# Optimization experiments

Measured on AMD Instinct MI355X. Metric: run time of the kernel, lower is better.

Reference implementation:

```python
import jax, jax.numpy as jnp
import numpy as np

T = 32            # timesteps
DT = 1e-3
TAU_MEM_INV = 100.0   # norse LIFParameters / LIParameters default (1/1e-2)
TAU_SYN_INV = 200.0   # default (1/5e-3)
V_TH = 1.0
ALPHA = 100.0         # superspike surrogate slope

@jax.custom_vjp
def heaviside(x):
    return (x > 0).astype(x.dtype)

def _h_fwd(x):
    return heaviside(x), x

def _h_bwd(x, g):
    # superspike surrogate gradient
    return (g / (ALPHA * jnp.abs(x) + 1.0) ** 2,)

heaviside.defvjp(_h_fwd, _h_bwd)

LAYER_SIZES = [(2000, 12000), (1500, 2000), (1000, 1500), (500, 1000), (100, 500), (10, 100)]

def setup_inputs() -> dict:
    key = jax.random.key(0)
    ks = jax.random.split(key, 7)
    B = 128
    images = jax.random.normal(ks[0], (B, 3, 40, 100), dtype=jnp.float32)
    inp = {"images": images}
    for i, (out_f, in_f) in enumerate(LAYER_SIZES):
        scale = float(np.sqrt(2.0 / in_f))
        inp[f"w{i}"] = jax.random.normal(ks[i + 1], (out_f, in_f), dtype=jnp.float32) * scale
    return inp

def _encode(x):
    # norse ConstantCurrentLIFEncoder / lif_current_encode: voltage-only LIF
    def step(v, _):
        v = v + DT * TAU_MEM_INV * (-v + x)
        z = heaviside(v - V_TH)
        v = v - z * v  # v_reset = 0
        return v, z
    _, spikes = jax.lax.scan(step, jnp.zeros_like(x), None, length=T)
    return spikes  # [T, B, F]

def _lif_step(state, inp):
    # norse lif_feed_forward_step (parameter-free LIFCell)
    v, i = state
    v_dec = v + DT * TAU_MEM_INV * (-v + i)
    i_dec = i * (1.0 - DT * TAU_SYN_INV)
    z = heaviside(v_dec - V_TH)
    v_new = (1.0 - z) * v_dec  # v_reset = 0
    return (v_new, i_dec + inp), z

def _li_step(state, inp, w):
    # norse LILinearCell li_step (no bias)
    v, i = state
    i_jump = i + inp @ w.T
    v_new = v + DT * TAU_MEM_INV * (-v + i_jump)
    i_new = i_jump * (1.0 - DT * TAU_SYN_INV)
    return (v_new, i_new), v_new

def _forward(images, ws):
    B = images.shape[0]
    x = images.reshape(B, -1)  # [B, F]
    spikes = _encode(x)        # [T, B, F]
    lif_dims = [x.shape[1]] + [s[0] for s in LAYER_SIZES[:-1]]
    init_lif = tuple((jnp.zeros((B, d), x.dtype), jnp.zeros((B, d), x.dtype)) for d in lif_dims)
    init_li = tuple((jnp.zeros((B, s[0]), x.dtype), jnp.zeros((B, s[0]), x.dtype)) for s in LAYER_SIZES)

    def step(carry, s):
        lifs, lis = carry
        z = s
        new_lifs, new_lis = [], []
        for k in range(6):
            st, z = _lif_step(lifs[k], z)
            new_lifs.append(st)
            st2, z = _li_step(lis[k], z, ws[k])
            new_lis.append(st2)
        return (tuple(new_lifs), tuple(new_lis)), z

    _, outs = jax.lax.scan(step, (init_lif, init_li), spikes)  # [T, B, 10]
    out = jnp.max(outs, axis=0)
    return jax.nn.log_softmax(out, axis=1)

def reference(images, w0, w1, w2, w3, w4, w5):
    return _forward(images, (w0, w1, w2, w3, w4, w5))
```

## Files before the change

kernel.cpp:

```cpp
#include <hip/hip_runtime.h>

typedef _Float16 f16;
typedef _Float16 f16x2 __attribute__((ext_vector_type(2)));
typedef _Float16 f16x4 __attribute__((ext_vector_type(4)));
typedef _Float16 f16x8 __attribute__((ext_vector_type(8)));
typedef float f32x4 __attribute__((ext_vector_type(4)));
typedef unsigned int uint;

#define KM 0.1f
#define KS 0.8f
#define AS1 __attribute__((address_space(1)))
#define AS3 __attribute__((address_space(3)))
#define EPS_LO 2.44140625e-4f
#define KCAP0 2560
#define KCAP1 2048
#define KCAP2 1024

__global__ void enc_flags(const float* __restrict__ img, uint* __restrict__ Z,
                          uint* __restrict__ flagsB, uint* __restrict__ flags12, int n12) {
  if (blockIdx.x == 0) {
    for (int i = threadIdx.x; i < n12; i += 256) flags12[i] = 0u;
  }
  int idx = blockIdx.x * 256 + threadIdx.x;
  if (idx >= 128 * 3000) return;
  int b = idx / 3000, f = (idx - b * 3000) << 2;
  float4 t4 = *(const float4*)&img[b * 12000 + f];
  float x[4] = {t4.x, t4.y, t4.z, t4.w};
  float ve[4] = {0.f, 0.f, 0.f, 0.f}, vl[4] = {0.f, 0.f, 0.f, 0.f}, il[4] = {0.f, 0.f, 0.f, 0.f};
  uint m[4] = {0u, 0u, 0u, 0u};
  for (int t = 0; t < 32; ++t) {
#pragma unroll
    for (int e = 0; e < 4; ++e) {
      ve[e] = ve[e] + KM * (x[e] - ve[e]);
      float z0 = (ve[e] > 1.0f) ? 1.f : 0.f;
      ve[e] -= z0 * ve[e];
      float vd = vl[e] + KM * (il[e] - vl[e]);
      float id = KS * il[e];
      float z1 = (vd > 1.0f) ? 1.f : 0.f;
      m[e] |= (vd > 1.0f) ? (1u << t) : 0u;
      vl[e] = (1.f - z1) * vd;
      il[e] = id + z0;
    }
  }
  *(uint4*)&Z[b * 12032 + f] = make_uint4(m[0], m[1], m[2], m[3]);
  uint mask = 0u;
#pragma unroll
  for (int e = 0; e < 4; ++e) mask |= (m[e] ? 1u : 0u) << ((f & 31) + e);
  int lane = threadIdx.x & 63;
#pragma unroll
  for (int s = 1; s < 8; s <<= 1) mask |= (uint)__shfl_xor((int)mask, s);
  if ((lane & 7) == 0) flagsB[b * 375 + (f >> 5)] = mask;
}

__global__ void scan_cols(const uint* __restrict__ flagsIn, int* __restrict__ colidxOut,
                          int* __restrict__ metaOut, int nwords, int cstride, int cap,
                          int rows, int rowstride) {
  __shared__ int cnt[512];
  int g = blockIdx.x;
  int* colidx = colidxOut + g * cstride;
  int* meta = metaOut + g * 2;
  int t = threadIdx.x;
  uint w = 0u;
  if (t < nwords) {
    const uint* base = flagsIn + (size_t)g * rows * rowstride + t;
    for (int r = 0; r < rows; ++r) w |= base[r * rowstride];
  }
  cnt[t] = __popc(w);
  __syncthreads();
  for (int off = 1; off < 512; off <<= 1) {
    int v = cnt[t];
    int u = (t >= off) ? cnt[t - off] : 0;
    __syncthreads();
    cnt[t] = v + u;
    __syncthreads();
  }
  int base = cnt[t] - __popc(w);
  uint ww = w;
  int r = 0;
  while (ww) {
    int p = __ffs(ww) - 1;
    colidx[base + r] = t * 32 + p;
    ww &= ww - 1;
    ++r;
  }
  if (t == 511) {
    int K = cnt[511];
    if (K > cap) K = cap;
    meta[0] = K;
    meta[1] = (K + 63) & ~63;
  }
}

struct PrepArgs {
  const float* W[3];
  f16* dst[3];
  int Nr[3], Kr[3], Kp[3], Npd[3];
  int boff[4];
};

__global__ __launch_bounds__(512) void prep0_all(const float* __restrict__ W,
                                                 f16* __restrict__ W0g,
                                                 const uint* __restrict__ Z,
                                                 f16* __restrict__ Ag,
                                                 const int* __restrict__ colidx,
                                                 const int* __restrict__ meta,
                                                 PrepArgs pa) {
  __shared__ float row[12032];
  int blk = blockIdx.x;
  int tid = threadIdx.x;

  if (blk < 2048) {
    int o = blk;
    bool live = (o < 2000);
    if (live) {
      for (int f4 = tid * 4; f4 < 12000; f4 += 2048)
        *(float4*)&row[f4] = *(const float4*)&W[(size_t)o * 12000 + f4];
    }
    __syncthreads();
    int r2 = ((o >> 4) << 5) + (o & 15);
    for (int g = 0; g < 8; ++g) {
      int K = meta[g * 2], Kpc = meta[g * 2 + 1];
      const int* cidx = colidx + g * 12032;
      f16* dh = W0g + g * ((size_t)4096 * KCAP0) + (size_t)r2 * Kpc;
      f16* dl = W0g + g * ((size_t)4096 * KCAP0) + (size_t)(r2 + 16) * Kpc;
      for (int j = tid; j < Kpc; j += 512) {
        float w = (live && j < K) ? row[cidx[j]] : 0.f;
        f16 h = (f16)w;
        float hf = (float)h;
        if (__builtin_fabsf(hf) < 6.103515625e-05f) { h = (f16)0.f; hf = 0.f; }
        dh[j] = h;
        dl[j] = (f16)((w - hf) * 4096.0f);
      }
    }
    return;
  }

  if (blk < 3072) {
    int lb = blk - 2048;
    int g = lb >> 7, xb = lb & 127;
    int K = meta[g * 2], Kpc = meta[g * 2 + 1];
    if (Kpc == 0) return;
    const int* cidx = colidx + g * 12032;
    int j8n = Kpc >> 3;
    int total = 512 * j8n;
    for (int i = xb * 512 + tid; i < total; i += 128 * 512) {
      int r = i / j8n, j8 = (i - r * j8n) << 3;
      int b = g * 16 + (r >> 5), t = r & 31;
      f16x8 s;
#pragma unroll
      for (int e = 0; e < 8; ++e) {
        int j = j8 + e;
        uint m = (j < K) ? Z[b * 12032 + cidx[j]] : 0u;
        s[e] = (f16)(float)((m >> t) & 1u);
      }
      *(f16x8*)&Ag[g * ((size_t)512 * KCAP0) + (size_t)r * Kpc + j8] = s;
    }
    return;
  }

  {
    int lb = blk - 3072;
    int k = 0;
#pragma unroll
    for (int j = 0; j < 2; ++j) k += (lb >= pa.boff[j + 1]) ? 1 : 0;
    int i = (lb - pa.boff[k]) * 512 + tid;
    int Kp = pa.Kp[k];
    int kp4 = Kp >> 2;
    int total4 = pa.Npd[k] * kp4;
    if (i >= total4) return;
    int o = i / kp4, f = (i - o * kp4) << 2;
    float w[4] = {0.f, 0.f, 0.f, 0.f};
    if (o < pa.Nr[k] && f < pa.Kr[k]) {
      float4 t = *(const float4*)&pa.W[k][(size_t)o * pa.Kr[k] + f];
      w[0] = t.x; w[1] = t.y; w[2] = t.z; w[3] = t.w;
    }
    f16x4 h4, l4;
#pragma unroll
    for (int e = 0; e < 4; ++e) {
      f16 h = (f16)w[e];
      float hf = (float)h;
      if (__builtin_fabsf(hf) < 6.103515625e-05f) { h = (f16)0.f; hf = 0.f; }
      h4[e] = h;
      l4[e] = (f16)((w[e] - hf) * 4096.0f);
    }
    int r2 = ((o >> 4) << 5) + (o & 15);
    *(f16x4*)&pa.dst[k][(size_t)r2 * Kp + f] = h4;
    *(f16x4*)&pa.dst[k][(size_t)(r2 + 16) * Kp + f] = l4;
  }
}

__global__ __launch_bounds__(512) void prepk_all(const f16* __restrict__ src,
                                                 f16* __restrict__ dst,
                                                 const float* __restrict__ W,
                                                 f16* __restrict__ Wg,
                                                 const int* __restrict__ colidx,
                                                 const int* __restrict__ meta,
                                                 int srcW, int cstride, size_t astr,
                                                 int Nr, int Kr, size_t bstr) {
  __shared__ float row[2048];
  int blk = blockIdx.x;
  int tid = threadIdx.x;

  if (blk < 4096) {
    int r = blk;
    int g = r >> 9;
    int K = meta[g * 2], Kpc = meta[g * 2 + 1];
    if (Kpc == 0) return;
    const int* cidx = colidx + g * cstride;
    const f16* s = src + (size_t)r * srcW;
    f16* d = dst + g * astr + (size_t)(r & 511) * Kpc;
    for (int j = tid; j < Kpc; j += 512)
      d[j] = (j < K) ? s[cidx[j]] : (f16)0.f;
    return;
  }

  {
    int o = blk - 4096;
    bool live = (o < Nr);
    if (live) {
      for (int f4 = tid * 4; f4 < Kr; f4 += 2048)
        *(float4*)&row[f4] = *(const float4*)&W[(size_t)o * Kr + f4];
    }
    __syncthreads();
    int r2 = ((o >> 4) << 5) + (o & 15);
    for (int g = 0; g < 8; ++g) {
      int K = meta[g * 2], Kpc = meta[g * 2 + 1];
      const int* cidx = colidx + g * cstride;
      f16* dh = Wg + g * bstr + (size_t)r2 * Kpc;
      f16* dl = Wg + g * bstr + (size_t)(r2 + 16) * Kpc;
      for (int j = tid; j < Kpc; j += 512) {
        float w = 0.f;
        if (live && j < K) {
          int c = cidx[j];
          w = (c < Kr) ? row[c] : 0.f;
        }
        f16 h = (f16)w;
        float hf = (float)h;
        if (__builtin_fabsf(hf) < 6.103515625e-05f) { h = (f16)0.f; hf = 0.f; }
        dh[j] = h;
        dl[j] = (f16)((w - hf) * 4096.0f);
      }
    }
  }
}

template <int WM>
__global__ __launch_bounds__(WM * 128, 4)
void gemm_fused(const f16* __restrict__ A, const f16* __restrict__ B2,
                f16* __restrict__ Spk, float* __restrict__ Out,
                const int* __restrict__ kpcp, int KpFixed, int Np,
                uint* __restrict__ colFlags, int cfw, int grouped,
                size_t astr, size_t bstr) {
  constexpr int BM = WM * 64;
  constexpr int NT = WM * 128;
  constexpr int BI = 1024 / NT;
  __shared__ f16 smem[BM * 64 + 128 * 64];
  f16* sA = smem;
  f16* sB = smem + BM * 64;
  const int tid = threadIdx.x;
  const int lane = tid & 63;
  const int wave = tid >> 6;
  const int wr = wave >> 1;
  const int wc = wave & 1;

  const int nx = gridDim.x;
  const int flat = blockIdx.y * nx + blockIdx.x;
  const int cpx = (nx * gridDim.y) >> 3;
  const int id = (flat & 7) * cpx + (flat >> 3);
  const int m0 = (id / nx) * BM;
  const int n0 = (id % nx) * 128;

  int Kp;
  size_t aoff, boff;
  if (grouped) {
    int g = m0 >> 9;
    Kp = kpcp[g * 2 + 1];
    aoff = g * astr + (size_t)(m0 & 511) * Kp;
    boff = g * bstr + (size_t)n0 * Kp;
  } else {
    Kp = kpcp ? kpcp[1] : KpFixed;
    aoff = (size_t)m0 * Kp;
    boff = (size_t)n0 * Kp;
  }

  f32x4 zero = {0.f, 0.f, 0.f, 0.f};
  f32x4 acc[4][4];
#pragma unroll
  for (int m = 0; m < 4; ++m)
#pragma unroll
    for (int n = 0; n < 4; ++n) acc[m][n] = zero;

  const f16* Abase = A + aoff;
  const f16* Bbase = B2 + boff;
  const int nkt = Kp >> 6;
  for (int kt = 0; kt < nkt; ++kt) {
    __syncthreads();
    const f16* Ab = Abase + (size_t)kt * 64;
    const f16* Bb = Bbase + (size_t)kt * 64;
#pragma unroll
    for (int j = 0; j < 4; ++j) {
      int q = j * NT + tid;
      int r = q >> 3, c = ((q & 7) ^ (r & 7)) * 8;
      __builtin_amdgcn_global_load_lds((const AS1 void*)(Ab + (size_t)r * Kp + c),
                                       (AS3 void*)(&sA[q * 8]), 16, 0, 0);
    }
#pragma unroll
    for (int j = 0; j < BI; ++j) {
      int q = j * NT + tid;
      int r = q >> 3, c = ((q & 7) ^ (r & 7)) * 8;
      __builtin_amdgcn_global_load_lds((const AS1 void*)(Bb + (size_t)r * Kp + c),
                                       (AS3 void*)(&sB[q * 8]), 16, 0, 0);
    }
    __syncthreads();
#pragma unroll
    for (int kk = 0; kk < 2; ++kk) {
      const int lr = lane & 15;
      const int hq = lane >> 4;
      f16x8 af[4], bf[4];
#pragma unroll
      for (int m = 0; m < 4; ++m) {
        int R = wr * 64 + m * 16 + lr;
        int ch = (kk * 4 + hq) ^ (R & 7);
        af[m] = *(const f16x8*)&sA[R * 64 + ch * 8];
      }
#pragma unroll
      for (int n = 0; n < 4; ++n) {
        int R = wc * 64 + n * 16 + lr;
        int ch = (kk * 4 + hq) ^ (R & 7);
        bf[n] = *(const f16x8*)&sB[R * 64 + ch * 8];
      }
#pragma unroll
      for (int m = 0; m < 4; ++m)
#pragma unroll
        for (int n = 0; n < 4; ++n)
          acc[m][n] = __builtin_amdgcn_mfma_f32_16x16x32_f16(af[m], bf[n], acc[m][n], 0, 0, 0);
    }
  }

  const int lr = lane & 15, lq = lane >> 4;
  float* scr = (float*)smem + wave * 1152;
  const int baseRow = m0 + wr * 64;

  if (Out) {
    __syncthreads();
#pragma unroll
    for (int m = 0; m < 4; ++m)
#pragma unroll
      for (int i = 0; i < 4; ++i)
        scr[(m * 16 + lq * 4 + i) * 17 + lr] = acc[m][0][i] + EPS_LO * acc[m][1][i];
    __syncthreads();
    float mx = -3.4e38f;
    if (lane < 32) {
      int bl = lane >> 4, c = lane & 15;
      float vL = 0.f, iL = 0.f;
      for (int t = 0; t < 32; ++t) {
        float g = scr[(bl * 32 + t) * 17 + c];
        float ij = iL + g;
        vL = vL + KM * (ij - vL);
        iL = KS * ij;
        mx = fmaxf(mx, vL);
      }
    }
    float v = (lane < 32 && (lane & 15) < 10) ? mx : -3.4e38f;
    float M = v;
#pragma unroll
    for (int s = 1; s < 16; s <<= 1) M = fmaxf(M, __shfl_xor(M, s));
    float e = (lane < 32 && (lane & 15) < 10) ? expf(v - M) : 0.f;
    float sum = e;
#pragma unroll
    for (int s = 1; s < 16; s <<= 1) sum += __shfl_xor(sum, s);
    if (n0 == 0 && wc == 0 && lane < 32 && (lane & 15) < 10) {
      int b = (baseRow >> 5) + (lane >> 4);
      Out[b * 10 + (lane & 15)] = v - M - logf(sum);
    }
    return;
  }

  __syncthreads();
#pragma unroll
  for (int h = 0; h < 2; ++h) {
#pragma unroll
    for (int m = 0; m < 4; ++m)
#pragma unroll
      for (int i = 0; i < 4; ++i)
        scr[(m * 16 + lq * 4 + i) * 17 + lr] = acc[m][2 * h][i] + EPS_LO * acc[m][2 * h + 1][i];
    __syncthreads();
    if (lane < 32) {
      int bl = lane >> 4, c = lane & 15;
      float vL = 0.f, iL = 0.f, vF = 0.f, iF = 0.f;
      for (int t = 0; t < 32; ++t) {
        float g = scr[(bl * 32 + t) * 17 + c];
        float ij = iL + g;
        vL = vL + KM * (ij - vL);
        iL = KS * ij;
        float vd = vF + KM * (iF - vF);
        float idec = KS * iF;
        float z = (vd > 1.0f) ? 1.f : 0.f;
        vF = (1.f - z) * vd;
        iF = idec + vL;
        scr[(bl * 32 + t) * 17 + c] = z;
      }
    }
    __syncthreads();
    {
      int row = lane;
      f16x8 v0, v1;
#pragma unroll
      for (int cc = 0; cc < 8; ++cc) {
        v0[cc] = (f16)scr[row * 17 + cc];
        v1[cc] = (f16)scr[row * 17 + 8 + cc];
      }
      size_t go = (size_t)(baseRow + row) * Np + (n0 >> 1) + wc * 32 + h * 16;
      *(f16x8*)&Spk[go] = v0;
      *(f16x8*)&Spk[go + 8] = v1;
      if (colFlags) {
        uint bits = 0u;
#pragma unroll
        for (int cc = 0; cc < 8; ++cc) {
          bits |= (__any((float)v0[cc] != 0.f) ? 1u : 0u) << cc;
          bits |= (__any((float)v1[cc] != 0.f) ? 1u : 0u) << (8 + cc);
        }
        int cstart = (n0 >> 1) + wc * 32 + h * 16;
        int g1 = baseRow >> 9;
        if (lane == 0 && bits)
          atomicOr(&colFlags[g1 * cfw + (cstart >> 5)], bits << (cstart & 31));
      }
    }
    __syncthreads();
  }
}

extern "C" void kernel_launch(void* const* d_in, const int* in_sizes, int n_in,
                              void* d_out, int out_size, void* d_ws, size_t ws_size,
                              hipStream_t stream) {
  const float* img = (const float*)d_in[0];

  char* p = (char*)d_ws;
  f16* W0g = (f16*)p; p += 8 * (size_t)4096 * KCAP0 * 2;
  f16* W1g = (f16*)p; p += 8 * (size_t)3072 * KCAP1 * 2;
  f16* W2g = (f16*)p; p += 8 * (size_t)2048 * KCAP2 * 2;
  f16* W3 = (f16*)p;  p += (size_t)2 * 512 * 1024 * 2;
  f16* W4 = (f16*)p;  p += (size_t)2 * 128 * 512 * 2;
  f16* W5 = (f16*)p;  p += (size_t)2 * 128 * 128 * 2;
  f16* Ag = (f16*)p;  p += 8 * (size_t)512 * KCAP0 * 2;
  f16* T0 = (f16*)p;  p += (size_t)4096 * 2048 * 2;
  f16* T1 = (f16*)p;  p += (size_t)4096 * 2048 * 2;
  uint* Z = (uint*)p; p += (size_t)128 * 12032 * 4;
  uint* flagsB = (uint*)p; p += (size_t)128 * 375 * 4;
  uint* flags1 = (uint*)p; p += 8 * 64 * 4;
  uint* flags2 = (uint*)p; p += 8 * 48 * 4;
  int* colidx = (int*)p;  p += 8 * 12032 * 4;
  int* colidx1 = (int*)p; p += 8 * 2048 * 4;
  int* colidx2 = (int*)p; p += 8 * 1536 * 4;
  int* meta = (int*)p;  p += 16 * 4;
  int* meta1 = (int*)p; p += 16 * 4;
  int* meta2 = (int*)p; p += 16 * 4;

  enc_flags<<<(128 * 3000 + 255) / 256, 256, 0, stream>>>(img, Z, flagsB, flags1,
                                                          8 * 64 + 8 * 48);
  scan_cols<<<8, 512, 0, stream>>>(flagsB, colidx, meta, 375, 12032, KCAP0, 16, 375);

  PrepArgs pa;
  static const int Nr3[3] = {500, 100, 10}, Kr3[3] = {1000, 500, 100};
  static const int Kp3[3] = {1024, 512, 128}, Np3[3] = {512, 128, 128};
  f16* dst3[3] = {W3, W4, W5};
  int nb = 0;
  for (int k = 0; k < 3; ++k) {
    pa.W[k] = (const float*)d_in[k + 4];
    pa.dst[k] = dst3[k];
    pa.Nr[k] = Nr3[k]; pa.Kr[k] = Kr3[k]; pa.Kp[k] = Kp3[k]; pa.Npd[k] = Np3[k];
    pa.boff[k] = nb;
    nb += ((Np3[k] * Kp3[k]) >> 2) / 512;
  }
  pa.boff[3] = nb;
  prep0_all<<<3072 + nb, 512, 0, stream>>>((const float*)d_in[1], W0g, Z, Ag,
                                           colidx, meta, pa);

  gemm_fused<4><<<dim3(32, 16), dim3(512), 0, stream>>>(
      Ag, W0g, T0, nullptr, meta, 0, 2048, flags1, 64, 1,
      (size_t)512 * KCAP0, (size_t)4096 * KCAP0);

  scan_cols<<<8, 512, 0, stream>>>(flags1, colidx1, meta1, 64, 2048, KCAP1, 1, 64);
  prepk_all<<<4096 + 1536, 512, 0, stream>>>(T0, T1, (const float*)d_in[2], W1g,
                                             colidx1, meta1, 2048, 2048,
                                             (size_t)512 * KCAP1, 1500, 2000,
                                             (size_t)3072 * KCAP1);

  gemm_fused<4><<<dim3(24, 16), dim3(512), 0, stream>>>(
      T1, W1g, T0, nullptr, meta1, 0, 1536, flags2, 48, 1,
      (size_t)512 * KCAP1, (size_t)3072 * KCAP1);

  scan_cols<<<8, 512, 0, stream>>>(flags2, colidx2, meta2, 48, 1536, KCAP2, 1, 48);
  prepk_all<<<4096 + 1024, 512, 0, stream>>>(T0, T1, (const float*)d_in[3], W2g,
                                             colidx2, meta2, 1536, 1536,
                                             (size_t)512 * KCAP2, 1000, 1500,
                                             (size_t)2048 * KCAP2);

  gemm_fused<2><<<dim3(16, 32), dim3(256), 0, stream>>>(
      T1, W2g, T0, nullptr, meta2, 0, 1024, nullptr, 0, 1,
      (size_t)512 * KCAP2, (size_t)2048 * KCAP2);

  gemm_fused<2><<<dim3(8, 32), dim3(256), 0, stream>>>(
      T0, W3, T1, nullptr, nullptr, 1024, 512, nullptr, 0, 0, 0, 0);
  gemm_fused<2><<<dim3(2, 32), dim3(256), 0, stream>>>(
      T1, W4, T0, nullptr, nullptr, 512, 128, nullptr, 0, 0, 0, 0);
  gemm_fused<2><<<dim3(2, 32), dim3(256), 0, stream>>>(
      T0, W5, nullptr, (float*)d_out, nullptr, 128, 128, nullptr, 0, 0, 0, 0);
}
```

Measured before the change: 154.5 us.

## Extend sparse active-column compaction to layer 3 and retile layer-1 GEMM

Layer 2's GEMM now writes column-activity flags. A new scan_cols and prepk_all pass compacts the active spike columns for layer 3, and its weights are gathered into per-group packed buffers, so the layer-3 GEMM runs over only the active K instead of the dense 1024. Layer 3's weight conversion is removed from the shared prep kernel. The layer-1 GEMM also switches from 4-wave 512-thread tiles to 2-wave 256-thread tiles with twice as many blocks. This adds two kernel launches and extra gather traffic, which may cost more than the skipped work at this small layer size.

```diff
diff --git a/kernel.cpp b/kernel.cpp
--- a/kernel.cpp
+++ b/kernel.cpp
@@ -15,11 +15,12 @@
 #define KCAP0 2560
 #define KCAP1 2048
 #define KCAP2 1024
+#define KCAP3 1024
 
 __global__ void enc_flags(const float* __restrict__ img, uint* __restrict__ Z,
-                          uint* __restrict__ flagsB, uint* __restrict__ flags12, int n12) {
+                          uint* __restrict__ flagsB, uint* __restrict__ flags123, int n123) {
   if (blockIdx.x == 0) {
-    for (int i = threadIdx.x; i < n12; i += 256) flags12[i] = 0u;
+    for (int i = threadIdx.x; i < n123; i += 256) flags123[i] = 0u;
   }
   int idx = blockIdx.x * 256 + threadIdx.x;
   if (idx >= 128 * 3000) return;
@@ -92,10 +93,10 @@
 }
 
 struct PrepArgs {
-  const float* W[3];
-  f16* dst[3];
-  int Nr[3], Kr[3], Kp[3], Npd[3];
-  int boff[4];
+  const float* W[2];
+  f16* dst[2];
+  int Nr[2], Kr[2], Kp[2], Npd[2];
+  int boff[3];
 };
 
 __global__ __launch_bounds__(512) void prep0_all(const float* __restrict__ W,
@@ -160,9 +161,7 @@
 
   {
     int lb = blk - 3072;
-    int k = 0;
-#pragma unroll
-    for (int j = 0; j < 2; ++j) k += (lb >= pa.boff[j + 1]) ? 1 : 0;
+    int k = (lb >= pa.boff[1]) ? 1 : 0;
     int i = (lb - pa.boff[k]) * 512 + tid;
     int Kp = pa.Kp[k];
     int kp4 = Kp >> 2;
@@ -439,7 +438,7 @@
   f16* W0g = (f16*)p; p += 8 * (size_t)4096 * KCAP0 * 2;
   f16* W1g = (f16*)p; p += 8 * (size_t)3072 * KCAP1 * 2;
   f16* W2g = (f16*)p; p += 8 * (size_t)2048 * KCAP2 * 2;
-  f16* W3 = (f16*)p;  p += (size_t)2 * 512 * 1024 * 2;
+  f16* W3g = (f16*)p; p += 8 * (size_t)1024 * KCAP3 * 2;
   f16* W4 = (f16*)p;  p += (size_t)2 * 128 * 512 * 2;
   f16* W5 = (f16*)p;  p += (size_t)2 * 128 * 128 * 2;
   f16* Ag = (f16*)p;  p += 8 * (size_t)512 * KCAP0 * 2;
@@ -449,30 +448,33 @@
   uint* flagsB = (uint*)p; p += (size_t)128 * 375 * 4;
   uint* flags1 = (uint*)p; p += 8 * 64 * 4;
   uint* flags2 = (uint*)p; p += 8 * 48 * 4;
+  uint* flags3 = (uint*)p; p += 8 * 32 * 4;
   int* colidx = (int*)p;  p += 8 * 12032 * 4;
   int* colidx1 = (int*)p; p += 8 * 2048 * 4;
   int* colidx2 = (int*)p; p += 8 * 1536 * 4;
+  int* colidx3 = (int*)p; p += 8 * 1024 * 4;
   int* meta = (int*)p;  p += 16 * 4;
   int* meta1 = (int*)p; p += 16 * 4;
   int* meta2 = (int*)p; p += 16 * 4;
+  int* meta3 = (int*)p; p += 16 * 4;
 
   enc_flags<<<(128 * 3000 + 255) / 256, 256, 0, stream>>>(img, Z, flagsB, flags1,
-                                                          8 * 64 + 8 * 48);
+                                                          8 * 64 + 8 * 48 + 8 * 32);
   scan_cols<<<8, 512, 0, stream>>>(flagsB, colidx, meta, 375, 12032, KCAP0, 16, 375);
 
   PrepArgs pa;
-  static const int Nr3[3] = {500, 100, 10}, Kr3[3] = {1000, 500, 100};
-  static const int Kp3[3] = {1024, 512, 128}, Np3[3] = {512, 128, 128};
-  f16* dst3[3] = {W3, W4, W5};
+  static const int Nr2[2] = {100, 10}, Kr2[2] = {500, 100};
+  static const int Kp2[2] = {512, 128}, Np2[2] = {128, 128};
+  f16* dst2[2] = {W4, W5};
   int nb = 0;
-  for (int k = 0; k < 3; ++k) {
-    pa.W[k] = (const float*)d_in[k + 4];
-    pa.dst[k] = dst3[k];
-    pa.Nr[k] = Nr3[k]; pa.Kr[k] = Kr3[k]; pa.Kp[k] = Kp3[k]; pa.Npd[k] = Np3[k];
+  for (int k = 0; k < 2; ++k) {
+    pa.W[k] = (const float*)d_in[k + 5];
+    pa.dst[k] = dst2[k];
+    pa.Nr[k] = Nr2[k]; pa.Kr[k] = Kr2[k]; pa.Kp[k] = Kp2[k]; pa.Npd[k] = Np2[k];
     pa.boff[k] = nb;
-    nb += ((Np3[k] * Kp3[k]) >> 2) / 512;
-  }
-  pa.boff[3] = nb;
+    nb += ((Np2[k] * Kp2[k]) >> 2) / 512;
+  }
+  pa.boff[2] = nb;
   prep0_all<<<3072 + nb, 512, 0, stream>>>((const float*)d_in[1], W0g, Z, Ag,
                                            colidx, meta, pa);
 
@@ -486,7 +488,7 @@
                                              (size_t)512 * KCAP1, 1500, 2000,
                                              (size_t)3072 * KCAP1);
 
-  gemm_fused<4><<<dim3(24, 16), dim3(512), 0, stream>>>(
+  gemm_fused<2><<<dim3(24, 32), dim3(256), 0, stream>>>(
       T1, W1g, T0, nullptr, meta1, 0, 1536, flags2, 48, 1,
       (size_t)512 * KCAP1, (size_t)3072 * KCAP1);
 
@@ -497,13 +499,21 @@
                                              (size_t)2048 * KCAP2);
 
   gemm_fused<2><<<dim3(16, 32), dim3(256), 0, stream>>>(
-      T1, W2g, T0, nullptr, meta2, 0, 1024, nullptr, 0, 1,
+      T1, W2g, T0, nullptr, meta2, 0, 1024, flags3, 32, 1,
       (size_t)512 * KCAP2, (size_t)2048 * KCAP2);
 
+  scan_cols<<<8, 512, 0, stream>>>(flags3, colidx3, meta3, 32, 1024, KCAP3, 1, 32);
+  prepk_all<<<4096 + 512, 512, 0, stream>>>(T0, T1, (const float*)d_in[4], W3g,
+                                            colidx3, meta3, 1024, 1024,
+                                            (size_t)512 * KCAP3, 500, 1000,
+                                            (size_t)1024 * KCAP3);
+
   gemm_fused<2><<<dim3(8, 32), dim3(256), 0, stream>>>(
-      T0, W3, T1, nullptr, nullptr, 1024, 512, nullptr, 0, 0, 0, 0);
+      T1, W3g, T0, nullptr, meta3, 0, 512, nullptr, 0, 1,
+      (size_t)512 * KCAP3, (size_t)1024 * KCAP3);
+
   gemm_fused<2><<<dim3(2, 32), dim3(256), 0, stream>>>(
-      T1, W4, T0, nullptr, nullptr, 512, 128, nullptr, 0, 0, 0, 0);
+      T0, W4, T1, nullptr, nullptr, 512, 128, nullptr, 0, 0, 0, 0);
   gemm_fused<2><<<dim3(2, 32), dim3(256), 0, stream>>>(
-      T0, W5, nullptr, (float*)d_out, nullptr, 128, 128, nullptr, 0, 0, 0, 0);
+      T1, W5, nullptr, (float*)d_out, nullptr, 128, 128, nullptr, 0, 0, 0, 0);
 }
```

New measurement: 143.6 us. -7.1%, faster.
